# Optimization experiments

Hardware: AMD Instinct MI355X
Metric: run time of the kernel (lower is better)

The kernel has to match this reference:

```python
import jax, jax.numpy as jnp
import numpy as np
from jax import lax

EPS = 1e-5
NEG_SLOPE = 0.1
RES_SCALE = float(np.sqrt(0.5))


def upsample2x(x):
    # bilinear, align_corners=False (half-pixel), matches torch nn.Upsample(mode='bilinear')
    B, C, H, W = x.shape
    return jax.image.resize(x, (B, C, 2 * H, 2 * W), method='bilinear')


def modulated_conv2d(x, weight, styles, eps=EPS):
    # x: [B, I, H, W]; weight: [O, I, kh, kw]; styles: [B, I]
    B, I, H, W = x.shape
    O, _, kh, kw = weight.shape
    wmod = weight[None] * styles[:, None, :, None, None]            # [B,O,I,kh,kw]
    demod = lax.rsqrt(jnp.sum(wmod * wmod, axis=(2, 3, 4)) + eps)   # [B,O]
    wmod = wmod * demod[:, :, None, None, None]
    x_g = x.reshape(1, B * I, H, W)
    w_g = wmod.reshape(B * O, I, kh, kw)
    out = lax.conv_general_dilated(
        x_g, w_g, window_strides=(1, 1), padding=[(1, 1), (1, 1)],
        feature_group_count=B,
        dimension_numbers=('NCHW', 'OIHW', 'NCHW'))
    return out.reshape(B, O, H, W)


def style_block(x, w, n, conv_w, A_w, A_b, B_w, B_b, upsample):
    if upsample:
        x = upsample2x(x)
    scores = w @ A_w.T + A_b                      # [B, in_ch]
    x = modulated_conv2d(x, conv_w, scores)
    noise = n @ B_w.T + B_b                        # [B, out_ch]
    x = x + noise[:, :, None, None]
    return jnp.where(x >= 0, x, NEG_SLOPE * x)     # LeakyReLU(0.1)


def setup_inputs() -> dict:
    key = jax.random.key(0)
    ks = jax.random.split(key, 16)
    Bn, Ci, Co, Wd, Nd, H = 8, 256, 128, 512, 512, 64
    s = lambda k, shape, scale=0.05: jax.random.normal(k, shape, jnp.float32) * scale
    return {
        'x': jax.random.normal(ks[0], (Bn, Ci, H, H), jnp.float32),
        'w': jax.random.normal(ks[1], (Bn, Wd), jnp.float32),
        'n': jax.random.normal(ks[2], (Bn, Nd), jnp.float32),
        'rgb': jax.random.normal(ks[3], (Bn, 3, H, H), jnp.float32),
        'conv1_w': s(ks[4], (Ci, Ci, 3, 3)),
        'A1_w': s(ks[5], (Ci, Wd)), 'A1_b': jnp.ones((Ci,), jnp.float32),
        'B1_w': s(ks[6], (Ci, Nd)), 'B1_b': jnp.zeros((Ci,), jnp.float32),
        'conv2_w': s(ks[7], (Co, Ci, 3, 3)),
        'A2_w': s(ks[8], (Ci, Wd)), 'A2_b': jnp.ones((Ci,), jnp.float32),
        'B2_w': s(ks[9], (Co, Nd)), 'B2_b': jnp.zeros((Co,), jnp.float32),
        'rgb_w': s(ks[10], (3, Co, 1, 1)),
        'rgb_b': jnp.zeros((3,), jnp.float32),
    }


def reference(x, w, n, rgb, conv1_w, A1_w, A1_b, B1_w, B1_b,
              conv2_w, A2_w, A2_b, B2_w, B2_b, rgb_w, rgb_b):
    x = style_block(x, w, n, conv1_w, A1_w, A1_b, B1_w, B1_b, upsample=False)
    x = style_block(x, w, n, conv2_w, A2_w, A2_b, B2_w, B2_b, upsample=True)
    to_rgb = lax.conv_general_dilated(
        x, rgb_w, (1, 1), padding=[(0, 0), (0, 0)],
        dimension_numbers=('NCHW', 'OIHW', 'NCHW')) + rgb_b[None, :, None, None]
    rgb_out = (to_rgb + upsample2x(rgb)) * RES_SCALE
    return x, rgb_out
```

## Files before the change

### kernel.cpp

```cpp
#include <hip/hip_runtime.h>
#include <math.h>

#define BN 8
#define C1 256
#define C2 128
#define WD 512

typedef float  f32x4  __attribute__((ext_vector_type(4)));
typedef short  bf16x8 __attribute__((ext_vector_type(8)));
typedef unsigned short ushort_t;
typedef ushort_t us8 __attribute__((ext_vector_type(8)));
typedef ushort_t us4 __attribute__((ext_vector_type(4)));

__device__ __forceinline__ int clampi(int v, int lo, int hi) {
    return v < lo ? lo : (v > hi ? hi : v);
}
__device__ __forceinline__ float bf2f(ushort_t u) {
    return __uint_as_float(((unsigned int)u) << 16);
}
__device__ __forceinline__ ushort_t f2bf(float f) {
    unsigned int u = __float_as_uint(f);
    u = (u + 0x7fff + ((u >> 16) & 1)) >> 16;
    return (ushort_t)u;
}

__global__ __launch_bounds__(256)
void affine_kernel(const float* __restrict__ w, const float* __restrict__ n,
                   const float* __restrict__ A1w, const float* __restrict__ A1b,
                   const float* __restrict__ B1w, const float* __restrict__ B1b,
                   const float* __restrict__ A2w, const float* __restrict__ A2b,
                   const float* __restrict__ B2w, const float* __restrict__ B2b,
                   float* __restrict__ s1, float* __restrict__ s2,
                   float* __restrict__ n1, float* __restrict__ n2) {
    int tid = threadIdx.x;
    int gw = blockIdx.x * 4 + (tid >> 6);
    int lane = tid & 63;
    if (gw >= BN * 896) return;
    int b = gw / 896;
    int j = gw % 896;
    const float* vec; const float* M; const float* bias; float* out; int o;
    if (j < 256)      { o = j;       vec = w + b * WD; M = A1w; bias = A1b; out = s1 + b * 256; }
    else if (j < 512) { o = j - 256; vec = w + b * WD; M = A2w; bias = A2b; out = s2 + b * 256; }
    else if (j < 768) { o = j - 512; vec = n + b * WD; M = B1w; bias = B1b; out = n1 + b * 256; }
    else              { o = j - 768; vec = n + b * WD; M = B2w; bias = B2b; out = n2 + b * 128; }
    const float* row = M + (size_t)o * WD;
    int k0 = lane * 8;
    float4 v0 = *(const float4*)(vec + k0), v1 = *(const float4*)(vec + k0 + 4);
    float4 r0 = *(const float4*)(row + k0), r1 = *(const float4*)(row + k0 + 4);
    float acc = v0.x*r0.x + v0.y*r0.y + v0.z*r0.z + v0.w*r0.w
              + v1.x*r1.x + v1.y*r1.y + v1.z*r1.z + v1.w*r1.w;
    #pragma unroll
    for (int m = 1; m < 64; m <<= 1) acc += __shfl_xor(acc, m, 64);
    if (lane == 0) out[o] = acc + bias[o];
}

__global__ __launch_bounds__(256)
void demod_kernel(const float* __restrict__ cw1, const float* __restrict__ cw2,
                  const float* __restrict__ s1, const float* __restrict__ s2,
                  float* __restrict__ d1, float* __restrict__ d2) {
    int tid = threadIdx.x;
    int gw = blockIdx.x * 4 + (tid >> 6);
    int lane = tid & 63;
    if (gw >= BN * 384) return;
    int b = gw / 384;
    int j = gw % 384;
    const float* wbase; const float* s; float* dout; int o;
    if (j < 256) { o = j;       wbase = cw1; s = s1 + b * 256; dout = d1 + b * 256; }
    else         { o = j - 256; wbase = cw2; s = s2 + b * 256; dout = d2 + b * 128; }
    float acc = 0.f;
    #pragma unroll
    for (int i = 0; i < 4; i++) {
        int ic = lane * 4 + i;
        float sv = s[ic]; sv *= sv;
        const float* wk = wbase + ((size_t)o * 256 + ic) * 9;
        float t = 0.f;
        #pragma unroll
        for (int k = 0; k < 9; k++) t += wk[k] * wk[k];
        acc += t * sv;
    }
    #pragma unroll
    for (int m = 1; m < 64; m <<= 1) acc += __shfl_xor(acc, m, 64);
    if (lane == 0) dout[o] = rsqrtf(acc + 1e-5f);
}

__global__ __launch_bounds__(256)
void wprep_kernel(const float* __restrict__ cw1, const float* __restrict__ cw2,
                  ushort_t* __restrict__ wT1, ushort_t* __restrict__ wT2) {
    int idx = blockIdx.x * 256 + threadIdx.x;
    if (idx < 9 * 256 * 256) {
        int tap = idx >> 16;
        int oc = (idx >> 8) & 255;
        int ic = idx & 255;
        wT1[idx] = f2bf(cw1[((size_t)(oc * 256 + ic)) * 9 + tap]);
    } else if (idx < 9 * 256 * 256 + 9 * 128 * 256) {
        int e = idx - 9 * 256 * 256;
        int tap = e >> 15;
        int oc = (e >> 8) & 127;
        int ic = e & 255;
        wT2[e] = f2bf(cw2[((size_t)(oc * 256 + ic)) * 9 + tap]);
    }
}

__global__ __launch_bounds__(512)
void xprep_kernel(const float* __restrict__ x, const float* __restrict__ s1,
                  ushort_t* __restrict__ xTp) {
    int tid = threadIdx.x;
    int b = blockIdx.y;
    int px_lin = blockIdx.x * 16 + (tid >> 5);
    int ic8 = tid & 31;
    int gy = px_lin >> 6, gx = px_lin & 63;
    const float* xb = x + (((size_t)b * C1) << 12) + (gy << 6) + gx;
    float4 slo = *(const float4*)(s1 + b * 256 + ic8 * 8);
    float4 shi = *(const float4*)(s1 + b * 256 + ic8 * 8 + 4);
    float sv[8] = {slo.x, slo.y, slo.z, slo.w, shi.x, shi.y, shi.z, shi.w};
    us8 h;
    #pragma unroll
    for (int j = 0; j < 8; j++) {
        float v = xb[((size_t)(ic8 * 8 + j)) << 12];
        h[j] = f2bf(v * sv[j]);
    }
    *(us8*)(xTp + (size_t)b * 66 * 66 * 256 + ((size_t)(gy + 1) * 66 + gx + 1) * 256 + ic8 * 8) = h;
}

__global__ __launch_bounds__(256)
void upsample_kernel(const ushort_t* __restrict__ y1T, const float* __restrict__ s2,
                     ushort_t* __restrict__ y1up) {
    int flat = blockIdx.x * 256 + threadIdx.x;
    int b = blockIdx.y;
    int ic8 = flat & 31;
    int pxl = flat >> 5;
    int ux = pxl & 127, uy = pxl >> 7;
    int jyA; float wyA;
    if (uy & 1) { jyA = uy >> 1;       wyA = 0.75f; }
    else        { jyA = (uy >> 1) - 1; wyA = 0.25f; }
    int jxA; float wxA;
    if (ux & 1) { jxA = ux >> 1;       wxA = 0.75f; }
    else        { jxA = (ux >> 1) - 1; wxA = 0.25f; }
    int yA = clampi(jyA, 0, 63), yB = clampi(jyA + 1, 0, 63);
    int xA = clampi(jxA, 0, 63), xB = clampi(jxA + 1, 0, 63);
    float wyB = 1.f - wyA, wxB = 1.f - wxA;
    const ushort_t* yb = y1T + (size_t)b * 64 * 64 * 256 + ic8 * 8;
    us8 qAA = *(const us8*)(yb + (size_t)(yA * 64 + xA) * 256);
    us8 qAB = *(const us8*)(yb + (size_t)(yA * 64 + xB) * 256);
    us8 qBA = *(const us8*)(yb + (size_t)(yB * 64 + xA) * 256);
    us8 qBB = *(const us8*)(yb + (size_t)(yB * 64 + xB) * 256);
    float4 slo = *(const float4*)(s2 + b * 256 + ic8 * 8);
    float4 shi = *(const float4*)(s2 + b * 256 + ic8 * 8 + 4);
    float sv[8] = {slo.x, slo.y, slo.z, slo.w, shi.x, shi.y, shi.z, shi.w};
    us8 h;
    #pragma unroll
    for (int j = 0; j < 8; j++) {
        float v = wyA * (wxA * bf2f(qAA[j]) + wxB * bf2f(qAB[j]))
                + wyB * (wxA * bf2f(qBA[j]) + wxB * bf2f(qBB[j]));
        h[j] = f2bf(v * sv[j]);
    }
    *(us8*)(y1up + (size_t)b * 130 * 130 * 256 + ((size_t)(uy + 1) * 130 + ux + 1) * 256 + ic8 * 8) = h;
}

template<int ROWSTR, int OCTOT, int OUTW, int TPR, bool IS_CONV2>
__global__ __launch_bounds__(256, 2)
void conv_mfma(const ushort_t* __restrict__ inp, const ushort_t* __restrict__ wT,
               const float* __restrict__ dmod, const float* __restrict__ nza,
               ushort_t* __restrict__ outT,
               const float* __restrict__ rgb_in, const float* __restrict__ rw,
               const float* __restrict__ rb, float* __restrict__ xout,
               float* __restrict__ rgbo) {
    __shared__ __align__(16) ushort_t actS[18 * 18 * 32];
    __shared__ __align__(16) ushort_t wS[9 * 64 * 32];
    int b = blockIdx.z, ocg = blockIdx.y, tile = blockIdx.x;
    int tyT = tile / TPR, txT = tile % TPR;
    int ty0 = tyT * 16, tx0 = txT * 16;
    int tid = threadIdx.x, lane = tid & 63, wave = tid >> 6;
    int col = lane & 15, quad = lane >> 4;

    const ushort_t* inb = inp + (size_t)b * ROWSTR * ROWSTR * 256;

    int actOff[6]; bool actOk[6];
    #pragma unroll
    for (int i = 0; i < 6; i++) {
        int u = tid + 256 * i;
        actOk[i] = (u < 1296);
        int pxl = u >> 2, ic8 = u & 3;
        int py = pxl / 18, px = pxl - py * 18;
        actOff[i] = ((ty0 + py) * ROWSTR + tx0 + px) * 256 + ic8 * 8;
    }
    int wOff[9];
    #pragma unroll
    for (int i = 0; i < 9; i++) {
        int u = tid + 256 * i;
        int tap = u >> 8, oc = (u >> 2) & 63, ic8 = u & 3;
        wOff[i] = (tap * OCTOT + ocg * 64 + oc) * 256 + ic8 * 8;
    }

    us8 aReg[6], wReg[9];
#define LOADK(KC) { \
    _Pragma("unroll") for (int i = 0; i < 6; i++) \
        if (actOk[i]) aReg[i] = *(const us8*)(inb + actOff[i] + (KC) * 32); \
    _Pragma("unroll") for (int i = 0; i < 9; i++) \
        wReg[i] = *(const us8*)(wT + wOff[i] + (KC) * 32); }
#define STOREK() { \
    _Pragma("unroll") for (int i = 0; i < 6; i++) \
        if (actOk[i]) *(us8*)(actS + (size_t)(tid + 256 * i) * 8) = aReg[i]; \
    _Pragma("unroll") for (int i = 0; i < 9; i++) \
        *(us8*)(wS + (size_t)(tid + 256 * i) * 8) = wReg[i]; }

    f32x4 acc[4][4];
    #pragma unroll
    for (int mt = 0; mt < 4; mt++)
        #pragma unroll
        for (int nt = 0; nt < 4; nt++) acc[mt][nt] = (f32x4)(0.f);

    LOADK(0);
    STOREK();
    __syncthreads();

    for (int kc = 0; kc < 8; kc++) {
        if (kc < 7) LOADK(kc + 1);
        #pragma unroll
        for (int tap = 0; tap < 9; tap++) {
            const int dy = tap / 3, dx = tap % 3;
            bf16x8 a[4], bb[4];
            #pragma unroll
            for (int mt = 0; mt < 4; mt++)
                a[mt] = *(const bf16x8*)(wS + ((tap * 64 + mt * 16 + col) * 32 + quad * 8));
            #pragma unroll
            for (int nt = 0; nt < 4; nt++)
                bb[nt] = *(const bf16x8*)(actS + (((4 * wave + nt + dy) * 18 + col + dx) * 32 + quad * 8));
            #pragma unroll
            for (int mt = 0; mt < 4; mt++)
                #pragma unroll
                for (int nt = 0; nt < 4; nt++)
                    acc[mt][nt] = __builtin_amdgcn_mfma_f32_16x16x32_bf16(a[mt], bb[nt], acc[mt][nt], 0, 0, 0);
        }
        __syncthreads();
        if (kc < 7) { STOREK(); }
        __syncthreads();
    }
#undef LOADK
#undef STOREK

    if (!IS_CONV2) {
        #pragma unroll
        for (int mt = 0; mt < 4; mt++) {
            int oc0 = ocg * 64 + mt * 16 + quad * 4;
            float4 dv = *(const float4*)(dmod + b * OCTOT + oc0);
            float4 nv = *(const float4*)(nza + b * OCTOT + oc0);
            float dva[4] = {dv.x, dv.y, dv.z, dv.w};
            float nva[4] = {nv.x, nv.y, nv.z, nv.w};
            #pragma unroll
            for (int nt = 0; nt < 4; nt++) {
                int gy = ty0 + 4 * wave + nt, gx = tx0 + col;
                us4 h;
                #pragma unroll
                for (int r = 0; r < 4; r++) {
                    float t = acc[mt][nt][r] * dva[r] + nva[r];
                    t = (t >= 0.f) ? t : 0.1f * t;
                    h[r] = f2bf(t);
                }
                *(us4*)(outT + ((size_t)b * OUTW * OUTW + gy * OUTW + gx) * 256 + oc0) = h;
            }
        }
    } else {
        float dva[4][4], nva[4][4], rwa[3][4][4];
        #pragma unroll
        for (int mt = 0; mt < 4; mt++) {
            int oc0 = ocg * 64 + mt * 16 + quad * 4;
            float4 dv = *(const float4*)(dmod + b * 128 + oc0);
            float4 nv = *(const float4*)(nza + b * 128 + oc0);
            dva[mt][0] = dv.x; dva[mt][1] = dv.y; dva[mt][2] = dv.z; dva[mt][3] = dv.w;
            nva[mt][0] = nv.x; nva[mt][1] = nv.y; nva[mt][2] = nv.z; nva[mt][3] = nv.w;
            #pragma unroll
            for (int c = 0; c < 3; c++) {
                float4 rv = *(const float4*)(rw + c * 128 + oc0);
                rwa[c][mt][0] = rv.x; rwa[c][mt][1] = rv.y; rwa[c][mt][2] = rv.z; rwa[c][mt][3] = rv.w;
            }
        }
        #pragma unroll
        for (int nt = 0; nt < 4; nt++) {
            int uy = ty0 + 4 * wave + nt, ux = tx0 + col;
            float pc0 = 0.f, pc1 = 0.f, pc2 = 0.f;
            #pragma unroll
            for (int mt = 0; mt < 4; mt++) {
                int oc0 = ocg * 64 + mt * 16 + quad * 4;
                #pragma unroll
                for (int r = 0; r < 4; r++) {
                    float t = acc[mt][nt][r] * dva[mt][r] + nva[mt][r];
                    t = (t >= 0.f) ? t : 0.1f * t;
                    xout[(((size_t)b * 128 + oc0 + r) << 14) + (uy << 7) + ux] = t;
                    pc0 += rwa[0][mt][r] * t;
                    pc1 += rwa[1][mt][r] * t;
                    pc2 += rwa[2][mt][r] * t;
                }
            }
            if (ocg == 0 && quad == 0) {
                int jyA; float wyA;
                if (uy & 1) { jyA = uy >> 1;       wyA = 0.75f; }
                else        { jyA = (uy >> 1) - 1; wyA = 0.25f; }
                int jxA; float wxA;
                if (ux & 1) { jxA = ux >> 1;       wxA = 0.75f; }
                else        { jxA = (ux >> 1) - 1; wxA = 0.25f; }
                int yA = clampi(jyA, 0, 63), yB = clampi(jyA + 1, 0, 63);
                int xA = clampi(jxA, 0, 63), xB = clampi(jxA + 1, 0, 63);
                float wyB = 1.f - wyA, wxB = 1.f - wxA;
                const float* rp3 = rgb_in + (((size_t)b * 3) << 12);
                float up[3];
                #pragma unroll
                for (int c = 0; c < 3; c++) {
                    const float* rc = rp3 + ((size_t)c << 12);
                    up[c] = wyA * (wxA * rc[(yA << 6) + xA] + wxB * rc[(yA << 6) + xB])
                          + wyB * (wxA * rc[(yB << 6) + xA] + wxB * rc[(yB << 6) + xB]);
                }
                pc0 += rb[0] + up[0];
                pc1 += rb[1] + up[1];
                pc2 += rb[2] + up[2];
            }
            const float S = 0.70710678118654752f;
            atomicAdd(rgbo + (((size_t)b * 3 + 0) << 14) + (uy << 7) + ux, pc0 * S);
            atomicAdd(rgbo + (((size_t)b * 3 + 1) << 14) + (uy << 7) + ux, pc1 * S);
            atomicAdd(rgbo + (((size_t)b * 3 + 2) << 14) + (uy << 7) + ux, pc2 * S);
        }
    }
}

extern "C" void kernel_launch(void* const* d_in, const int* in_sizes, int n_in,
                              void* d_out, int out_size, void* d_ws, size_t ws_size,
                              hipStream_t stream) {
    (void)in_sizes; (void)n_in; (void)out_size; (void)ws_size;
    const float* x     = (const float*)d_in[0];
    const float* w     = (const float*)d_in[1];
    const float* n     = (const float*)d_in[2];
    const float* rgb   = (const float*)d_in[3];
    const float* cw1   = (const float*)d_in[4];
    const float* A1w   = (const float*)d_in[5];
    const float* A1b   = (const float*)d_in[6];
    const float* B1w   = (const float*)d_in[7];
    const float* B1b   = (const float*)d_in[8];
    const float* cw2   = (const float*)d_in[9];
    const float* A2w   = (const float*)d_in[10];
    const float* A2b   = (const float*)d_in[11];
    const float* B2w   = (const float*)d_in[12];
    const float* B2b   = (const float*)d_in[13];
    const float* rgbw  = (const float*)d_in[14];
    const float* rgbb  = (const float*)d_in[15];

    char* ws = (char*)d_ws;
    float* s1 = (float*)(ws);
    float* s2 = (float*)(ws + 8192);
    float* d1 = (float*)(ws + 16384);
    float* d2 = (float*)(ws + 24576);
    float* n1 = (float*)(ws + 28672);
    float* n2 = (float*)(ws + 36864);
    ushort_t* wT1  = (ushort_t*)(ws + 40960);
    ushort_t* wT2  = (ushort_t*)(ws + 1220608);
    ushort_t* xTp  = (ushort_t*)(ws + 1810432);
    ushort_t* y1up = (ushort_t*)(ws + 19652608);
    ushort_t* y1T  = (ushort_t*)(ws + 88875008);

    float* xout = (float*)d_out;
    float* rgbo = xout + (size_t)BN * C2 * 128 * 128;

    hipMemsetAsync(xTp, 0, 17842176 + 69222400, stream);
    hipMemsetAsync(rgbo, 0, (size_t)BN * 3 * 128 * 128 * 4, stream);

    affine_kernel<<<1792, 256, 0, stream>>>(w, n, A1w, A1b, B1w, B1b, A2w, A2b, B2w, B2b,
                                            s1, s2, n1, n2);
    demod_kernel<<<768, 256, 0, stream>>>(cw1, cw2, s1, s2, d1, d2);
    wprep_kernel<<<(9 * 256 * 256 + 9 * 128 * 256 + 255) / 256, 256, 0, stream>>>(cw1, cw2, wT1, wT2);
    xprep_kernel<<<dim3(256, BN), 512, 0, stream>>>(x, s1, xTp);
    conv_mfma<66, 256, 64, 4, false><<<dim3(16, 4, BN), 256, 0, stream>>>(
        xTp, wT1, d1, n1, y1T, nullptr, nullptr, nullptr, nullptr, nullptr);
    upsample_kernel<<<dim3(2048, BN), 256, 0, stream>>>(y1T, s2, y1up);
    conv_mfma<130, 128, 128, 8, true><<<dim3(64, 2, BN), 256, 0, stream>>>(
        y1up, wT2, d2, n2, nullptr, rgb, rgbw, rgbb, xout, rgbo);
}
```

Before: 310.8 us.

## Read MFMA-fragment-ordered weights directly from global, double-buffer activations, drop memsets

Weights are pre-permuted into the exact per-lane MFMA fragment order so each wave loads its A operands straight from global/L2 instead of staging them through shared memory. This removes the weight LDS buffer and allows double-buffering the activation tile with one barrier per K chunk, with occupancy raised to 3 blocks. The prep and upsample kernels now write the zero padding borders themselves, so the large workspace memset is removed. The risk is that repeated global weight loads in the inner tap loop add latency and cache pressure, which could outweigh the saved LDS traffic.

```diff
diff --git a/kernel.cpp b/kernel.cpp
--- a/kernel.cpp
+++ b/kernel.cpp
@@ -85,91 +85,94 @@
 
 __global__ __launch_bounds__(256)
 void wprep_kernel(const float* __restrict__ cw1, const float* __restrict__ cw2,
-                  ushort_t* __restrict__ wT1, ushort_t* __restrict__ wT2) {
+                  ushort_t* __restrict__ wTf1, ushort_t* __restrict__ wTf2) {
     int idx = blockIdx.x * 256 + threadIdx.x;
-    if (idx < 9 * 256 * 256) {
-        int tap = idx >> 16;
-        int oc = (idx >> 8) & 255;
-        int ic = idx & 255;
-        wT1[idx] = f2bf(cw1[((size_t)(oc * 256 + ic)) * 9 + tap]);
-    } else if (idx < 9 * 256 * 256 + 9 * 128 * 256) {
-        int e = idx - 9 * 256 * 256;
-        int tap = e >> 15;
-        int oc = (e >> 8) & 127;
-        int ic = e & 255;
-        wT2[e] = f2bf(cw2[((size_t)(oc * 256 + ic)) * 9 + tap]);
-    }
-}
-
-__global__ __launch_bounds__(512)
+    if (idx < 589824) {
+        int j = idx & 7, quad = (idx >> 3) & 3, col = (idx >> 5) & 15;
+        int kc = (idx >> 9) & 7, ocRow = (idx >> 12) & 15, tap = idx >> 16;
+        int oc = ocRow * 16 + col, ic = kc * 32 + quad * 8 + j;
+        wTf1[idx] = f2bf(cw1[((size_t)oc * 256 + ic) * 9 + tap]);
+    } else if (idx < 589824 + 294912) {
+        int e = idx - 589824;
+        int j = e & 7, quad = (e >> 3) & 3, col = (e >> 5) & 15;
+        int kc = (e >> 9) & 7, ocRow = (e >> 12) & 7, tap = e >> 15;
+        int oc = ocRow * 16 + col, ic = kc * 32 + quad * 8 + j;
+        wTf2[e] = f2bf(cw2[((size_t)oc * 256 + ic) * 9 + tap]);
+    }
+}
+
+__global__ __launch_bounds__(256)
 void xprep_kernel(const float* __restrict__ x, const float* __restrict__ s1,
                   ushort_t* __restrict__ xTp) {
-    int tid = threadIdx.x;
     int b = blockIdx.y;
-    int px_lin = blockIdx.x * 16 + (tid >> 5);
-    int ic8 = tid & 31;
-    int gy = px_lin >> 6, gx = px_lin & 63;
-    const float* xb = x + (((size_t)b * C1) << 12) + (gy << 6) + gx;
-    float4 slo = *(const float4*)(s1 + b * 256 + ic8 * 8);
-    float4 shi = *(const float4*)(s1 + b * 256 + ic8 * 8 + 4);
-    float sv[8] = {slo.x, slo.y, slo.z, slo.w, shi.x, shi.y, shi.z, shi.w};
-    us8 h;
-    #pragma unroll
-    for (int j = 0; j < 8; j++) {
-        float v = xb[((size_t)(ic8 * 8 + j)) << 12];
-        h[j] = f2bf(v * sv[j]);
-    }
-    *(us8*)(xTp + (size_t)b * 66 * 66 * 256 + ((size_t)(gy + 1) * 66 + gx + 1) * 256 + ic8 * 8) = h;
+    int flat = blockIdx.x * 256 + threadIdx.x;
+    if (flat >= 66 * 66 * 32) return;
+    int ic8 = flat & 31, pxl = flat >> 5;
+    int gy = pxl / 66, gx = pxl - gy * 66;
+    us8 h = {0, 0, 0, 0, 0, 0, 0, 0};
+    if (gy >= 1 && gy <= 64 && gx >= 1 && gx <= 64) {
+        const float* xb = x + (((size_t)b * C1) << 12) + ((gy - 1) << 6) + (gx - 1);
+        float4 slo = *(const float4*)(s1 + b * 256 + ic8 * 8);
+        float4 shi = *(const float4*)(s1 + b * 256 + ic8 * 8 + 4);
+        float sv[8] = {slo.x, slo.y, slo.z, slo.w, shi.x, shi.y, shi.z, shi.w};
+        #pragma unroll
+        for (int j = 0; j < 8; j++) {
+            float v = xb[((size_t)(ic8 * 8 + j)) << 12];
+            h[j] = f2bf(v * sv[j]);
+        }
+    }
+    *(us8*)(xTp + (size_t)b * 66 * 66 * 256 + (size_t)pxl * 256 + ic8 * 8) = h;
 }
 
 __global__ __launch_bounds__(256)
 void upsample_kernel(const ushort_t* __restrict__ y1T, const float* __restrict__ s2,
                      ushort_t* __restrict__ y1up) {
+    int b = blockIdx.y;
     int flat = blockIdx.x * 256 + threadIdx.x;
-    int b = blockIdx.y;
-    int ic8 = flat & 31;
-    int pxl = flat >> 5;
-    int ux = pxl & 127, uy = pxl >> 7;
-    int jyA; float wyA;
-    if (uy & 1) { jyA = uy >> 1;       wyA = 0.75f; }
-    else        { jyA = (uy >> 1) - 1; wyA = 0.25f; }
-    int jxA; float wxA;
-    if (ux & 1) { jxA = ux >> 1;       wxA = 0.75f; }
-    else        { jxA = (ux >> 1) - 1; wxA = 0.25f; }
-    int yA = clampi(jyA, 0, 63), yB = clampi(jyA + 1, 0, 63);
-    int xA = clampi(jxA, 0, 63), xB = clampi(jxA + 1, 0, 63);
-    float wyB = 1.f - wyA, wxB = 1.f - wxA;
-    const ushort_t* yb = y1T + (size_t)b * 64 * 64 * 256 + ic8 * 8;
-    us8 qAA = *(const us8*)(yb + (size_t)(yA * 64 + xA) * 256);
-    us8 qAB = *(const us8*)(yb + (size_t)(yA * 64 + xB) * 256);
-    us8 qBA = *(const us8*)(yb + (size_t)(yB * 64 + xA) * 256);
-    us8 qBB = *(const us8*)(yb + (size_t)(yB * 64 + xB) * 256);
-    float4 slo = *(const float4*)(s2 + b * 256 + ic8 * 8);
-    float4 shi = *(const float4*)(s2 + b * 256 + ic8 * 8 + 4);
-    float sv[8] = {slo.x, slo.y, slo.z, slo.w, shi.x, shi.y, shi.z, shi.w};
-    us8 h;
-    #pragma unroll
-    for (int j = 0; j < 8; j++) {
-        float v = wyA * (wxA * bf2f(qAA[j]) + wxB * bf2f(qAB[j]))
-                + wyB * (wxA * bf2f(qBA[j]) + wxB * bf2f(qBB[j]));
-        h[j] = f2bf(v * sv[j]);
-    }
-    *(us8*)(y1up + (size_t)b * 130 * 130 * 256 + ((size_t)(uy + 1) * 130 + ux + 1) * 256 + ic8 * 8) = h;
-}
-
-template<int ROWSTR, int OCTOT, int OUTW, int TPR, bool IS_CONV2>
-__global__ __launch_bounds__(256, 2)
-void conv_mfma(const ushort_t* __restrict__ inp, const ushort_t* __restrict__ wT,
+    if (flat >= 130 * 130 * 32) return;
+    int ic8 = flat & 31, pxl = flat >> 5;
+    int uy0 = pxl / 130, ux0 = pxl - uy0 * 130;
+    us8 h = {0, 0, 0, 0, 0, 0, 0, 0};
+    if (uy0 >= 1 && uy0 <= 128 && ux0 >= 1 && ux0 <= 128) {
+        int uy = uy0 - 1, ux = ux0 - 1;
+        int jyA; float wyA;
+        if (uy & 1) { jyA = uy >> 1;       wyA = 0.75f; }
+        else        { jyA = (uy >> 1) - 1; wyA = 0.25f; }
+        int jxA; float wxA;
+        if (ux & 1) { jxA = ux >> 1;       wxA = 0.75f; }
+        else        { jxA = (ux >> 1) - 1; wxA = 0.25f; }
+        int yA = clampi(jyA, 0, 63), yB = clampi(jyA + 1, 0, 63);
+        int xA = clampi(jxA, 0, 63), xB = clampi(jxA + 1, 0, 63);
+        float wyB = 1.f - wyA, wxB = 1.f - wxA;
+        const ushort_t* yb = y1T + (size_t)b * 64 * 64 * 256 + ic8 * 8;
+        us8 qAA = *(const us8*)(yb + (size_t)(yA * 64 + xA) * 256);
+        us8 qAB = *(const us8*)(yb + (size_t)(yA * 64 + xB) * 256);
+        us8 qBA = *(const us8*)(yb + (size_t)(yB * 64 + xA) * 256);
+        us8 qBB = *(const us8*)(yb + (size_t)(yB * 64 + xB) * 256);
+        float4 slo = *(const float4*)(s2 + b * 256 + ic8 * 8);
+        float4 shi = *(const float4*)(s2 + b * 256 + ic8 * 8 + 4);
+        float sv[8] = {slo.x, slo.y, slo.z, slo.w, shi.x, shi.y, shi.z, shi.w};
+        #pragma unroll
+        for (int j = 0; j < 8; j++) {
+            float v = wyA * (wxA * bf2f(qAA[j]) + wxB * bf2f(qAB[j]))
+                    + wyB * (wxA * bf2f(qBA[j]) + wxB * bf2f(qBB[j]));
+            h[j] = f2bf(v * sv[j]);
+        }
+    }
+    *(us8*)(y1up + (size_t)b * 130 * 130 * 256 + (size_t)pxl * 256 + ic8 * 8) = h;
+}
+
+template<int ROWSTR, int OC16, int TPR, bool IS_CONV2>
+__global__ __launch_bounds__(256, 3)
+void conv_mfma(const ushort_t* __restrict__ inp, const ushort_t* __restrict__ wTf,
                const float* __restrict__ dmod, const float* __restrict__ nza,
                ushort_t* __restrict__ outT,
                const float* __restrict__ rgb_in, const float* __restrict__ rw,
                const float* __restrict__ rb, float* __restrict__ xout,
                float* __restrict__ rgbo) {
-    __shared__ __align__(16) ushort_t actS[18 * 18 * 32];
-    __shared__ __align__(16) ushort_t wS[9 * 64 * 32];
+    __shared__ __align__(16) ushort_t actS[2][18 * 18 * 32];
     int b = blockIdx.z, ocg = blockIdx.y, tile = blockIdx.x;
-    int tyT = tile / TPR, txT = tile % TPR;
-    int ty0 = tyT * 16, tx0 = txT * 16;
+    int ty0 = (tile / TPR) * 16, tx0 = (tile % TPR) * 16;
     int tid = threadIdx.x, lane = tid & 63, wave = tid >> 6;
     int col = lane & 15, quad = lane >> 4;
 
@@ -184,25 +187,15 @@
         int py = pxl / 18, px = pxl - py * 18;
         actOff[i] = ((ty0 + py) * ROWSTR + tx0 + px) * 256 + ic8 * 8;
     }
-    int wOff[9];
-    #pragma unroll
-    for (int i = 0; i < 9; i++) {
-        int u = tid + 256 * i;
-        int tap = u >> 8, oc = (u >> 2) & 63, ic8 = u & 3;
-        wOff[i] = (tap * OCTOT + ocg * 64 + oc) * 256 + ic8 * 8;
-    }
-
-    us8 aReg[6], wReg[9];
+    const ushort_t* wbase = wTf + (size_t)(ocg * 4) * 4096 + (col * 4 + quad) * 8;
+
+    us8 aReg[6];
 #define LOADK(KC) { \
     _Pragma("unroll") for (int i = 0; i < 6; i++) \
-        if (actOk[i]) aReg[i] = *(const us8*)(inb + actOff[i] + (KC) * 32); \
-    _Pragma("unroll") for (int i = 0; i < 9; i++) \
-        wReg[i] = *(const us8*)(wT + wOff[i] + (KC) * 32); }
-#define STOREK() { \
+        if (actOk[i]) aReg[i] = *(const us8*)(inb + actOff[i] + (KC) * 32); }
+#define STOREK(BUFI) { \
     _Pragma("unroll") for (int i = 0; i < 6; i++) \
-        if (actOk[i]) *(us8*)(actS + (size_t)(tid + 256 * i) * 8) = aReg[i]; \
-    _Pragma("unroll") for (int i = 0; i < 9; i++) \
-        *(us8*)(wS + (size_t)(tid + 256 * i) * 8) = wReg[i]; }
+        if (actOk[i]) *(us8*)(actS[BUFI] + (size_t)(tid + 256 * i) * 8) = aReg[i]; }
 
     f32x4 acc[4][4];
     #pragma unroll
@@ -211,29 +204,30 @@
         for (int nt = 0; nt < 4; nt++) acc[mt][nt] = (f32x4)(0.f);
 
     LOADK(0);
-    STOREK();
+    STOREK(0);
     __syncthreads();
 
     for (int kc = 0; kc < 8; kc++) {
+        int cur = kc & 1;
         if (kc < 7) LOADK(kc + 1);
+        const ushort_t* lb = actS[cur];
         #pragma unroll
         for (int tap = 0; tap < 9; tap++) {
             const int dy = tap / 3, dx = tap % 3;
             bf16x8 a[4], bb[4];
             #pragma unroll
             for (int mt = 0; mt < 4; mt++)
-                a[mt] = *(const bf16x8*)(wS + ((tap * 64 + mt * 16 + col) * 32 + quad * 8));
+                a[mt] = *(const bf16x8*)(wbase + (size_t)tap * OC16 * 4096 + mt * 4096 + kc * 512);
             #pragma unroll
             for (int nt = 0; nt < 4; nt++)
-                bb[nt] = *(const bf16x8*)(actS + (((4 * wave + nt + dy) * 18 + col + dx) * 32 + quad * 8));
+                bb[nt] = *(const bf16x8*)(lb + (((4 * wave + nt + dy) * 18 + col + dx) * 32 + quad * 8));
             #pragma unroll
             for (int mt = 0; mt < 4; mt++)
                 #pragma unroll
                 for (int nt = 0; nt < 4; nt++)
                     acc[mt][nt] = __builtin_amdgcn_mfma_f32_16x16x32_bf16(a[mt], bb[nt], acc[mt][nt], 0, 0, 0);
         }
-        __syncthreads();
-        if (kc < 7) { STOREK(); }
+        if (kc < 7) STOREK(cur ^ 1);
         __syncthreads();
     }
 #undef LOADK
@@ -243,8 +237,8 @@
         #pragma unroll
         for (int mt = 0; mt < 4; mt++) {
             int oc0 = ocg * 64 + mt * 16 + quad * 4;
-            float4 dv = *(const float4*)(dmod + b * OCTOT + oc0);
-            float4 nv = *(const float4*)(nza + b * OCTOT + oc0);
+            float4 dv = *(const float4*)(dmod + b * 256 + oc0);
+            float4 nv = *(const float4*)(nza + b * 256 + oc0);
             float dva[4] = {dv.x, dv.y, dv.z, dv.w};
             float nva[4] = {nv.x, nv.y, nv.z, nv.w};
             #pragma unroll
@@ -257,7 +251,7 @@
                     t = (t >= 0.f) ? t : 0.1f * t;
                     h[r] = f2bf(t);
                 }
-                *(us4*)(outT + ((size_t)b * OUTW * OUTW + gy * OUTW + gx) * 256 + oc0) = h;
+                *(us4*)(outT + (size_t)b * 64 * 64 * 256 + (size_t)(gy * 64 + gx) * 256 + oc0) = h;
             }
         }
     } else {
@@ -350,8 +344,8 @@
     float* d2 = (float*)(ws + 24576);
     float* n1 = (float*)(ws + 28672);
     float* n2 = (float*)(ws + 36864);
-    ushort_t* wT1  = (ushort_t*)(ws + 40960);
-    ushort_t* wT2  = (ushort_t*)(ws + 1220608);
+    ushort_t* wTf1 = (ushort_t*)(ws + 40960);
+    ushort_t* wTf2 = (ushort_t*)(ws + 1220608);
     ushort_t* xTp  = (ushort_t*)(ws + 1810432);
     ushort_t* y1up = (ushort_t*)(ws + 19652608);
     ushort_t* y1T  = (ushort_t*)(ws + 88875008);
@@ -359,17 +353,16 @@
     float* xout = (float*)d_out;
     float* rgbo = xout + (size_t)BN * C2 * 128 * 128;
 
-    hipMemsetAsync(xTp, 0, 17842176 + 69222400, stream);
     hipMemsetAsync(rgbo, 0, (size_t)BN * 3 * 128 * 128 * 4, stream);
 
     affine_kernel<<<1792, 256, 0, stream>>>(w, n, A1w, A1b, B1w, B1b, A2w, A2b, B2w, B2b,
                                             s1, s2, n1, n2);
     demod_kernel<<<768, 256, 0, stream>>>(cw1, cw2, s1, s2, d1, d2);
-    wprep_kernel<<<(9 * 256 * 256 + 9 * 128 * 256 + 255) / 256, 256, 0, stream>>>(cw1, cw2, wT1, wT2);
-    xprep_kernel<<<dim3(256, BN), 512, 0, stream>>>(x, s1, xTp);
-    conv_mfma<66, 256, 64, 4, false><<<dim3(16, 4, BN), 256, 0, stream>>>(
-        xTp, wT1, d1, n1, y1T, nullptr, nullptr, nullptr, nullptr, nullptr);
-    upsample_kernel<<<dim3(2048, BN), 256, 0, stream>>>(y1T, s2, y1up);
-    conv_mfma<130, 128, 128, 8, true><<<dim3(64, 2, BN), 256, 0, stream>>>(
-        y1up, wT2, d2, n2, nullptr, rgb, rgbw, rgbb, xout, rgbo);
-}
+    wprep_kernel<<<3456, 256, 0, stream>>>(cw1, cw2, wTf1, wTf2);
+    xprep_kernel<<<dim3((66 * 66 * 32 + 255) / 256, BN), 256, 0, stream>>>(x, s1, xTp);
+    conv_mfma<66, 16, 4, false><<<dim3(16, 4, BN), 256, 0, stream>>>(
+        xTp, wTf1, d1, n1, y1T, nullptr, nullptr, nullptr, nullptr, nullptr);
+    upsample_kernel<<<dim3((130 * 130 * 32 + 255) / 256, BN), 256, 0, stream>>>(y1T, s2, y1up);
+    conv_mfma<130, 8, 8, true><<<dim3(64, 2, BN), 256, 0, stream>>>(
+        y1up, wTf2, d2, n2, nullptr, rgb, rgbw, rgbb, xout, rgbo);
+}
```

Result: slower. 468.8 us (+50.8%).
